# Optimization experiments

Hardware: AMD Instinct MI355X
Metric: run time of the kernel (lower is better)

## Reference

```python
import jax, jax.numpy as jnp
import numpy as np
from jax import lax

V = 9; C1 = 80; C2 = 40; C4 = 24; CH = 32
H1, W1 = 30, 40; H2, W2 = 60, 80; H4, W4 = 120, 160
SHAPE = (96, 96, 96); N = 131072; EPS = 1e-5
OFFS = np.stack(np.meshgrid(np.arange(-1, 2), np.arange(-1, 2), np.arange(-1, 2), indexing='ij'), -1).reshape(-1, 3).astype(np.int32)  # 27 kernel offsets


def conv2d(x, w, b):
    y = lax.conv_general_dilated(x, w, (1, 1), 'SAME', dimension_numbers=('NCHW', 'OIHW', 'NCHW'))
    return y + b[None, :, None, None]


def bn1d(x, g, b):  # eval-mode BatchNorm1d (running_mean=0, running_var=1)
    return g * x * (1.0 / np.sqrt(1.0 + EPS)) + b


def layernorm(x, g, b):
    m = x.mean(-1, keepdims=True)
    v = ((x - m) ** 2).mean(-1, keepdims=True)
    return (x - m) / jnp.sqrt(v + EPS) * g + b


def grid_sample_zeros(img, gx, gy):
    # img [V,C,H,W]; gx,gy [V,M] normalized to [-1,1]; bilinear, align_corners=True, zeros padding
    Vn, C, H, W = img.shape
    px = (gx + 1.0) * 0.5 * (W - 1)
    py = (gy + 1.0) * 0.5 * (H - 1)
    x0 = jnp.floor(px); y0 = jnp.floor(py)
    wx = px - x0; wy = py - y0
    flat = img.reshape(Vn, C, H * W)
    def corner(xc, yc, wgt):
        valid = (xc >= 0) & (xc <= W - 1) & (yc >= 0) & (yc <= H - 1)
        xi = jnp.clip(xc, 0, W - 1).astype(jnp.int32)
        yi = jnp.clip(yc, 0, H - 1).astype(jnp.int32)
        idx = yi * W + xi  # [V,M]
        g = jax.vmap(lambda f, i: f[:, i])(flat, idx)  # [V,C,M]
        return g * (wgt * valid)[:, None, :]
    return (corner(x0, y0, (1 - wx) * (1 - wy)) + corner(x0 + 1, y0, wx * (1 - wy))
            + corner(x0, y0 + 1, (1 - wx) * wy) + corner(x0 + 1, y0 + 1, wx * wy))


def subm_conv(feat, W3, cxyz, grid):
    # submanifold sparse 3x3x3 conv: per-offset gather of active neighbors -> GEMM -> accumulate
    n = feat.shape[0]
    shp = jnp.asarray(SHAPE, jnp.int32)
    out = jnp.zeros((n, W3.shape[-1]), feat.dtype)
    for k in range(27):
        nc = cxyz + jnp.asarray(OFFS[k])
        inb = jnp.all((nc >= 0) & (nc < shp), axis=1)
        ncc = jnp.clip(nc, 0, shp - 1)
        idx = grid[ncc[:, 0], ncc[:, 1], ncc[:, 2]]
        ok = (inb & (idx >= 0)).astype(feat.dtype)
        g = feat[jnp.clip(idx, 0, n - 1)] * ok[:, None]
        out = out + g @ W3[k]
    return out


def _forward(feats_1x, feats_2x, feats_4x, origin, voxel_size, KRcam,
             w_f1, b_f1, w_f2, b_f2, w_f4, b_f4, w_down, b_down,
             w_p1, b_p1, w_p2, b_p2, w_p3, b_p3, w_p4, b_p4,
             bn0_g, bn0_b, w_elan, w_s1, ln1_g, ln1_b, w_s2, ln2_g, ln2_b,
             w_s3, ln3_g, ln3_b, w_s4, bn4_g, bn4_b,
             coords, stage, min_view_number):
    # feat_fusion_pre (bs=1, take batch 0)
    f1 = jax.nn.relu(conv2d(feats_1x[:, 0], w_f1, b_f1))
    f2 = jax.nn.relu(conv2d(feats_2x[:, 0], w_f2, b_f2))
    f4 = jax.nn.relu(conv2d(feats_4x[:, 0], w_f4, b_f4))
    f1 = jax.image.resize(f1, (V, C1, H2, W2), 'bilinear')  # F.interpolate x2
    f4 = f4.reshape(V, C4, H2, 2, W2, 2).mean(axis=(3, 5))  # AvgPool2d(2)
    fuse = jnp.concatenate([f1, f2, f4], axis=1)
    fuse = jax.nn.relu(conv2d(fuse, w_down, b_down))
    for w, b in ((w_p1, b_p1), (w_p2, b_p2), (w_p3, b_p3), (w_p4, b_p4)):
        fuse = fuse + jax.nn.relu(conv2d(fuse, w, b))  # residual blocks -> [V,CH,H2,W2]
    # multi-view projection
    cxyz = coords[:, 1:]
    world = cxyz.astype(jnp.float32) * voxel_size + origin[0]
    hom = jnp.concatenate([world, jnp.ones_like(world[:, :1])], axis=1)  # [N,4]
    im_p = jnp.einsum('vij,nj->vin', KRcam[:, 0], hom)  # [V,3,N]
    im_z = im_p[:, 2]
    gx = 2.0 * (im_p[:, 0] / im_z) / (W4 - 1) - 1.0
    gy = 2.0 * (im_p[:, 1] / im_z) / (H4 - 1) - 1.0
    mask = (jnp.abs(gx) <= 1) & (jnp.abs(gy) <= 1) & (im_z > 0)  # [V,N]
    count = mask.sum(0).astype(jnp.float32)
    # inputs are constructed so every voxel is seen by all views: valid_voxel compaction == identity
    feats = grid_sample_zeros(fuse, gx, gy) * mask[:, None, :]  # [V,CH,N]
    feat = feats.transpose(2, 0, 1)  # [N,V,CH]
    m = mask.T.astype(feat.dtype)  # [N,V]
    den = m.sum(1, keepdims=True)
    mean = (m[..., None] * feat).sum(1) / den
    var = (m[..., None] * (feat - mean[:, None, :]) ** 2).sum(1) / den  # [N,CH]
    # sparse subm conv chain
    sc = cxyz // (2 ** (2 - stage))  # stage=2 -> identity
    grid = jnp.full(SHAPE, -1, jnp.int32).at[sc[:, 0], sc[:, 1], sc[:, 2]].set(jnp.arange(N, dtype=jnp.int32))
    x = bn1d(var, bn0_g, bn0_b)
    x = jax.nn.relu(subm_conv(x, w_elan, sc, grid))  # Spares3dELAN stand-in
    r = jax.nn.relu(subm_conv(x, w_s1, sc, grid)); x = layernorm(r + x, ln1_g, ln1_b)
    r = jax.nn.relu(subm_conv(x, w_s2, sc, grid)); x = layernorm(r + x, ln2_g, ln2_b)
    r = jax.nn.relu(subm_conv(x, w_s3, sc, grid)); x = layernorm(r + x, ln3_g, ln3_b)
    occ = bn1d(subm_conv(x, w_s4, sc, grid), bn4_g, bn4_b)  # [N,1]
    return occ, coords, count


def setup_inputs() -> dict:
    key = jax.random.key(0)
    keys = jax.random.split(key, 40)
    ki = iter(range(40))
    def rn(shape, s=1.0):
        return jax.random.normal(keys[next(ki)], shape, jnp.float32) * s
    inp = {}
    inp['feats_1x'] = rn((V, 1, C1, H1, W1))
    inp['feats_2x'] = rn((V, 1, C2, H2, W2))
    inp['feats_4x'] = rn((V, 1, C4, H4, W4))
    flat = np.arange(N, dtype=np.int64) * 6  # unique active voxels in a 96^3 grid
    cx = flat // (96 * 96); rem = flat % (96 * 96)
    inp['coords'] = jnp.asarray(np.stack([np.zeros(N, np.int64), cx, rem // 96, rem % 96], 1), jnp.int32)
    inp['origin'] = jnp.asarray([[-1.92, -1.92, 1.0]], jnp.float32)
    inp['voxel_size'] = jnp.float32(0.04)
    fx, fy = 38.0, 28.0
    P = np.zeros((V, 1, 3, 4), np.float32)
    for v in range(V):
        P[v, 0] = np.array([[fx, 0.0, (W4 - 1) / 2, fx * 0.02 * (v - 4)],
                            [0.0, fy, (H4 - 1) / 2, 0.0],
                            [0.0, 0.0, 1.0, 0.0]], np.float32)
    inp['KRcam'] = jnp.asarray(P)
    s = 0.05
    inp['w_f1'] = rn((C1, C1, 3, 3), s); inp['b_f1'] = rn((C1,), s)
    inp['w_f2'] = rn((C2, C2, 3, 3), s); inp['b_f2'] = rn((C2,), s)
    inp['w_f4'] = rn((C4, C4, 3, 3), s); inp['b_f4'] = rn((C4,), s)
    inp['w_down'] = rn((CH, C1 + C2 + C4, 1, 1), s); inp['b_down'] = rn((CH,), s)
    for i in (1, 2, 3, 4):
        inp['w_p%d' % i] = rn((CH, CH, 3, 3), s); inp['b_p%d' % i] = rn((CH,), s)
    inp['bn0_g'] = jnp.ones((CH,), jnp.float32); inp['bn0_b'] = jnp.zeros((CH,), jnp.float32)
    inp['w_elan'] = rn((27, CH, CH), s)
    inp['w_s1'] = rn((27, CH, CH), s); inp['ln1_g'] = jnp.ones((CH,), jnp.float32); inp['ln1_b'] = jnp.zeros((CH,), jnp.float32)
    inp['w_s2'] = rn((27, CH, CH), s); inp['ln2_g'] = jnp.ones((CH,), jnp.float32); inp['ln2_b'] = jnp.zeros((CH,), jnp.float32)
    inp['w_s3'] = rn((27, CH, CH), s); inp['ln3_g'] = jnp.ones((CH,), jnp.float32); inp['ln3_b'] = jnp.zeros((CH,), jnp.float32)
    inp['w_s4'] = rn((27, CH, 1), s); inp['bn4_g'] = jnp.ones((1,), jnp.float32); inp['bn4_b'] = jnp.zeros((1,), jnp.float32)
    inp['stage'] = 2
    inp['min_view_number'] = 1
    return inp


def reference(feats_1x, feats_2x, feats_4x, origin, voxel_size, KRcam,
              w_f1, b_f1, w_f2, b_f2, w_f4, b_f4, w_down, b_down,
              w_p1, b_p1, w_p2, b_p2, w_p3, b_p3, w_p4, b_p4,
              bn0_g, bn0_b, w_elan, w_s1, ln1_g, ln1_b, w_s2, ln2_g, ln2_b,
              w_s3, ln3_g, ln3_b, w_s4, bn4_g, bn4_b,
              coords, stage, min_view_number):
    return _forward(feats_1x, feats_2x, feats_4x, origin, voxel_size, KRcam,
                    w_f1, b_f1, w_f2, b_f2, w_f4, b_f4, w_down, b_down,
                    w_p1, b_p1, w_p2, b_p2, w_p3, b_p3, w_p4, b_p4,
                    bn0_g, bn0_b, w_elan, w_s1, ln1_g, ln1_b, w_s2, ln2_g, ln2_b,
                    w_s3, ln3_g, ln3_b, w_s4, bn4_g, bn4_b,
                    coords, stage, min_view_number)
```

## Files before the change

### kernel.cpp

```cpp
#include <hip/hip_runtime.h>
#include <math.h>

#define VN 9
#define NVOX 131072
#define GS 96
static constexpr float INVS = 0.9999950000374997f;

typedef short bf16x8 __attribute__((ext_vector_type(8)));
typedef float f32x4v __attribute__((ext_vector_type(4)));

__device__ inline float4 ld4(const float* p){ return *reinterpret_cast<const float4*>(p); }

__device__ inline ushort f2b(float f){
  unsigned u = __float_as_uint(f);
  unsigned r = (u + 0x7fffu + ((u >> 16) & 1u)) >> 16;
  return (ushort)r;
}
__device__ inline float b2f(ushort s){ return __uint_as_float(((unsigned)s) << 16); }
__device__ inline float blo(unsigned u){ return __uint_as_float(u << 16); }
__device__ inline float bhi(unsigned u){ return __uint_as_float(u & 0xffff0000u); }

__device__ inline float4 ld4b(const ushort* p){
  uint2 u = *reinterpret_cast<const uint2*>(p);
  float4 r; r.x = blo(u.x); r.y = bhi(u.x); r.z = blo(u.y); r.w = bhi(u.y); return r;
}
__device__ inline void st4b(ushort* p, float4 v){
  uint2 u;
  u.x = (unsigned)f2b(v.x) | ((unsigned)f2b(v.y) << 16);
  u.y = (unsigned)f2b(v.z) | ((unsigned)f2b(v.w) << 16);
  *reinterpret_cast<uint2*>(p) = u;
}

__device__ inline void wprep2_dev(const float* __restrict__ w, ushort* __restrict__ o,
                                  int Cout, int Cin, int K, int CK, int CoutPad, int tid){
  int ci32 = tid & 31;
  int co = (tid >> 5) % CoutPad;
  int ck = (tid / (32*CoutPad)) % CK;
  int tap = tid / (32*CoutPad*CK);
  int ci = ck*32 + ci32;
  float v = 0.f;
  if (co < Cout && ci < Cin) v = w[(size_t)(co*Cin + ci)*K*K + tap];
  o[tid] = f2b(v);
}
__device__ inline void wprep_dev(const float* __restrict__ w, ushort* __restrict__ o, int tid){
  int k = tid >> 10;
  int r = tid & 1023;
  int co = r >> 5;
  int ci = r & 31;
  o[tid] = f2b(w[k*1024 + ci*32 + co]);
}

__device__ inline void nhwc_tile_dev(const float* __restrict__ in, ushort* __restrict__ out,
                                     int C, int Cpad, int HW, int tile, int tilesPerV,
                                     float* lds, int tx){
  int v  = tile / tilesPerV;
  int p0 = (tile - v*tilesPerV) * 64;
  const float* ip = in + (size_t)v*C*HW + p0;
  int iters = Cpad >> 2;
  for (int i = 0; i < iters; ++i){
    int idx = i*256 + tx;
    int c = idx >> 6;
    int p = idx & 63;
    float val = 0.f;
    if (c < C && (p0 + p) < HW) val = ip[(size_t)c*HW + p];
    lds[c*65 + p] = val;
  }
  __syncthreads();
  int groups = Cpad >> 2;
  int tot = 64*groups;
  for (int basei = 0; basei < tot; basei += 256){
    int idx = basei + tx;
    if (idx < tot){
      int g  = idx % groups;
      int px = idx / groups;
      if ((p0 + px) < HW){
        float4 r;
        r.x = lds[(g*4+0)*65 + px];
        r.y = lds[(g*4+1)*65 + px];
        r.z = lds[(g*4+2)*65 + px];
        r.w = lds[(g*4+3)*65 + px];
        st4b(out + (size_t)(v*HW + p0 + px)*Cpad + g*4, r);
      }
    }
  }
}

__global__ __launch_bounds__(256) void k_prep(
    const float* wf1s, const float* wf2s, const float* wf4s, const float* wdns,
    const float* wp0s, const float* wp1s, const float* wp2s, const float* wp3s,
    const float* wes, const float* ws1s, const float* ws2s, const float* ws3s,
    ushort* wf1, ushort* wf2, ushort* wf4, ushort* wdn,
    ushort* wp0, ushort* wp1, ushort* wp2, ushort* wp3,
    ushort* w2e, ushort* w2s1, ushort* w2s2, ushort* w2s3,
    int* grid,
    const float* f1, const float* f2, const float* f4,
    ushort* o1, ushort* o2, ushort* o4){
  __shared__ float lds[96*65];
  int bid = blockIdx.x;
  int tx = threadIdx.x;
  if (bid < 270){ int t = bid*256+tx; if (t < 69120) wprep2_dev(wf1s, wf1, 80, 80, 3, 3, 80, t); return; }
  bid -= 270;
  if (bid < 108){ int t = bid*256+tx; if (t < 27648) wprep2_dev(wf2s, wf2, 40, 40, 3, 2, 48, t); return; }
  bid -= 108;
  if (bid < 36){ int t = bid*256+tx; if (t < 9216) wprep2_dev(wf4s, wf4, 24, 24, 3, 1, 32, t); return; }
  bid -= 36;
  if (bid < 20){ int t = bid*256+tx; if (t < 5120) wprep2_dev(wdns, wdn, 32, 144, 1, 5, 32, t); return; }
  bid -= 20;
  if (bid < 36){ int t = bid*256+tx; if (t < 9216) wprep2_dev(wp0s, wp0, 32, 32, 3, 1, 32, t); return; }
  bid -= 36;
  if (bid < 36){ int t = bid*256+tx; if (t < 9216) wprep2_dev(wp1s, wp1, 32, 32, 3, 1, 32, t); return; }
  bid -= 36;
  if (bid < 36){ int t = bid*256+tx; if (t < 9216) wprep2_dev(wp2s, wp2, 32, 32, 3, 1, 32, t); return; }
  bid -= 36;
  if (bid < 36){ int t = bid*256+tx; if (t < 9216) wprep2_dev(wp3s, wp3, 32, 32, 3, 1, 32, t); return; }
  bid -= 36;
  if (bid < 108){ int t = bid*256+tx; if (t < 27648) wprep_dev(wes, w2e, t); return; }
  bid -= 108;
  if (bid < 108){ int t = bid*256+tx; if (t < 27648) wprep_dev(ws1s, w2s1, t); return; }
  bid -= 108;
  if (bid < 108){ int t = bid*256+tx; if (t < 27648) wprep_dev(ws2s, w2s2, t); return; }
  bid -= 108;
  if (bid < 108){ int t = bid*256+tx; if (t < 27648) wprep_dev(ws3s, w2s3, t); return; }
  bid -= 108;
  if (bid < 3456){ int t = bid*256+tx; if (t < GS*GS*GS) grid[t] = -1; return; }
  bid -= 3456;
  if (bid < 171){ nhwc_tile_dev(f1, o1, 80, 96, 1200, bid, 19, lds, tx); return; }
  bid -= 171;
  if (bid < 675){ nhwc_tile_dev(f2, o2, 40, 64, 4800, bid, 75, lds, tx); return; }
  bid -= 675;
  if (bid < 2700){ nhwc_tile_dev(f4, o4, 24, 32, 19200, bid, 300, lds, tx); }
}

template<int CK, int NT, int TAPS, int MT>
__device__ void conv_dev(
    const ushort* __restrict__ fin, const ushort* __restrict__ w2,
    const float* __restrict__ bias, ushort* __restrict__ outp,
    int H, int W, int total, int Cout, int outStride, int outOff,
    const ushort* __restrict__ skipin, int bid, int tid){
  constexpr int CIN = CK*32;
  constexpr int COP = NT*16;
  int lane = tid & 63;
  int wave = tid >> 6;
  int vbase = bid*(MT*64) + wave*(MT*16);
  int m = lane & 15, q = lane >> 4;
  int HW = H*W;
  int p[MT], py[MT], px[MT]; bool pin[MT];
  #pragma unroll
  for (int t = 0; t < MT; ++t){
    int pp = vbase + t*16 + m;
    pin[t] = pp < total;
    if (pp > total-1) pp = total-1;
    p[t] = pp;
    int v = pp / HW; int rem = pp - v*HW;
    int y = rem / W;
    py[t] = y; px[t] = rem - y*W;
  }
  f32x4v acc[MT][NT];
  #pragma unroll
  for (int t = 0; t < MT; ++t)
    #pragma unroll
    for (int n = 0; n < NT; ++n) acc[t][n] = 0.f;
  bf16x8 z = (short)0;

  #pragma unroll 1
  for (int tap = 0; tap < TAPS; ++tap){
    int dy = (TAPS == 9) ? tap/3 - 1 : 0;
    int dx = (TAPS == 9) ? tap%3 - 1 : 0;
    int off = dy*W + dx;
    bool val[MT];
    #pragma unroll
    for (int t = 0; t < MT; ++t)
      val[t] = pin[t] && ((unsigned)(py[t]+dy) < (unsigned)H)
                      && ((unsigned)(px[t]+dx) < (unsigned)W);
    #pragma unroll
    for (int ck = 0; ck < CK; ++ck){
      bf16x8 Af[MT], Bf[NT];
      #pragma unroll
      for (int t = 0; t < MT; ++t){
        size_t idx = val[t] ? (size_t)(p[t]+off) : 0;
        bf16x8 a = *(const bf16x8*)(fin + idx*CIN + ck*32 + q*8);
        Af[t] = val[t] ? a : z;
      }
      #pragma unroll
      for (int n = 0; n < NT; ++n)
        Bf[n] = *(const bf16x8*)(w2 + ((size_t)((tap*CK+ck)*COP + n*16 + m))*32 + q*8);
      #pragma unroll
      for (int t = 0; t < MT; ++t)
        #pragma unroll
        for (int n = 0; n < NT; ++n)
          acc[t][n] = __builtin_amdgcn_mfma_f32_16x16x32_bf16(Af[t], Bf[n], acc[t][n], 0, 0, 0);
    }
  }

  #pragma unroll
  for (int n = 0; n < NT; ++n){
    int co = n*16 + m;
    bool cok = co < Cout;
    float bs = cok ? bias[co] : 0.f;
    #pragma unroll
    for (int t = 0; t < MT; ++t){
      #pragma unroll
      for (int r = 0; r < 4; ++r){
        int pp = vbase + t*16 + q*4 + r;
        if (pp < total && cok){
          float x = fmaxf(acc[t][n][r] + bs, 0.f);
          if (skipin) x += b2f(skipin[(size_t)pp*CIN + co]);
          outp[(size_t)pp*outStride + outOff + co] = f2b(x);
        }
      }
    }
  }
}

template<int CK, int NT, int TAPS, int MT>
__global__ __launch_bounds__(256) void k_conv_mfma(
    const ushort* __restrict__ fin, const ushort* __restrict__ w2,
    const float* __restrict__ bias, ushort* __restrict__ outp,
    int H, int W, int total, int Cout, int outStride, int outOff,
    const ushort* __restrict__ skipin){
  conv_dev<CK,NT,TAPS,MT>(fin, w2, bias, outp, H, W, total, Cout, outStride, outOff,
                          skipin, blockIdx.x, threadIdx.x);
}

template<int TH, int NT>
__device__ void conv_lds_dev(
    const ushort* __restrict__ fin, const ushort* __restrict__ w2,
    const float* __restrict__ bias, ushort* __restrict__ outp,
    int H, int W, int Cout, int outStride,
    const ushort* __restrict__ skipin, ushort* lds, int bid, int tid){
  constexpr int RPW = TH/4;
  constexpr int PS = 36;
  int xtiles = W >> 4;
  int ytiles = (H + TH - 1) / TH;
  int v  = bid / (ytiles*xtiles);
  int rem = bid - v*(ytiles*xtiles);
  int ty = (rem / xtiles) * TH;
  int tx = (rem % xtiles) * 16;
  const ushort* ibase = fin + (size_t)v*H*W*32;
  for (int i = tid; i < (TH+2)*18*4; i += 256){
    int chunk = i & 3;
    int pxi = i >> 2;
    int ly = pxi / 18, lx = pxi - ly*18;
    int gy = ty + ly - 1, gx = tx + lx - 1;
    uint4 d = {0,0,0,0};
    if ((unsigned)gy < (unsigned)H && (unsigned)gx < (unsigned)W)
      d = *(const uint4*)(ibase + ((size_t)gy*W + gx)*32 + chunk*8);
    *(uint4*)(lds + (size_t)(ly*18 + lx)*PS + chunk*8) = d;
  }
  __syncthreads();
  int lane = tid & 63;
  int wave = tid >> 6;
  int m = lane & 15, q = lane >> 4;
  f32x4v acc[RPW][NT];
  #pragma unroll
  for (int t = 0; t < RPW; ++t)
    #pragma unroll
    for (int n = 0; n < NT; ++n) acc[t][n] = 0.f;

  #pragma unroll 1
  for (int tap = 0; tap < 9; ++tap){
    int dy = tap/3 - 1, dx = tap%3 - 1;
    bf16x8 Af[RPW], Bf[NT];
    #pragma unroll
    for (int t = 0; t < RPW; ++t){
      int ly = wave*RPW + t + 1 + dy;
      int lx = m + 1 + dx;
      Af[t] = *(const bf16x8*)(lds + (size_t)(ly*18 + lx)*PS + q*8);
    }
    #pragma unroll
    for (int n = 0; n < NT; ++n)
      Bf[n] = *(const bf16x8*)(w2 + ((size_t)(tap*(NT*16) + n*16 + m))*32 + q*8);
    #pragma unroll
    for (int t = 0; t < RPW; ++t)
      #pragma unroll
      for (int n = 0; n < NT; ++n)
        acc[t][n] = __builtin_amdgcn_mfma_f32_16x16x32_bf16(Af[t], Bf[n], acc[t][n], 0, 0, 0);
  }

  #pragma unroll
  for (int n = 0; n < NT; ++n){
    int co = n*16 + m;
    bool cok = co < Cout;
    float bs = cok ? bias[co] : 0.f;
    #pragma unroll
    for (int t = 0; t < RPW; ++t){
      int y = ty + wave*RPW + t;
      #pragma unroll
      for (int r = 0; r < 4; ++r){
        int x = tx + q*4 + r;
        if (y < H && cok){
          size_t pp = (size_t)(v*H + y)*W + x;
          float val = fmaxf(acc[t][n][r] + bs, 0.f);
          if (skipin) val += b2f(skipin[pp*32 + co]);
          outp[pp*outStride + co] = f2b(val);
        }
      }
    }
  }
}

__global__ __launch_bounds__(256) void k_conv_lds4(
    const ushort* __restrict__ fin, const ushort* __restrict__ w2,
    const float* __restrict__ bias, ushort* __restrict__ outp,
    const ushort* __restrict__ skipin){
  __shared__ ushort lds[6*18*36];
  conv_lds_dev<4,2>(fin, w2, bias, outp, 60, 80, 32, 32, skipin, lds, blockIdx.x, threadIdx.x);
}

__device__ void scatter_dev(const int* __restrict__ coords, const int* __restrict__ stage,
                            int* __restrict__ grid, int* __restrict__ scn,
                            float* __restrict__ coords_out,
                            const float* __restrict__ origin, const float* __restrict__ vsz,
                            const float* __restrict__ KR,
                            uint4* __restrict__ samp, float* __restrict__ cnt, int n){
  int c0 = coords[n*4], c1 = coords[n*4+1], c2 = coords[n*4+2], c3 = coords[n*4+3];
  coords_out[n*4+0] = (float)c0;
  coords_out[n*4+1] = (float)c1;
  coords_out[n*4+2] = (float)c2;
  coords_out[n*4+3] = (float)c3;
  int sh = 2 - stage[0];
  int s1 = c1 >> sh, s2 = c2 >> sh, s3 = c3 >> sh;
  scn[n*3+0] = s1; scn[n*3+1] = s2; scn[n*3+2] = s3;
  grid[(s1*GS + s2)*GS + s3] = n;

  float vs = vsz[0];
  float wx = (float)c1*vs + origin[0];
  float wy = (float)c2*vs + origin[1];
  float wz = (float)c3*vs + origin[2];
  float den = 0.f;
  #pragma unroll 1
  for (int v = 0; v < VN; ++v){
    const float* P = KR + v*12;
    float ix = P[0]*wx + P[1]*wy + P[2]*wz + P[3];
    float iy = P[4]*wx + P[5]*wy + P[6]*wz + P[7];
    float iz = P[8]*wx + P[9]*wy + P[10]*wz + P[11];
    float gx = 2.f*(ix/iz)/159.f - 1.f;
    float gy = 2.f*(iy/iz)/119.f - 1.f;
    bool ok = (fabsf(gx) <= 1.f) && (fabsf(gy) <= 1.f) && (iz > 0.f);
    float px = ok ? (gx + 1.f)*0.5f*79.f : 0.f;
    float py = ok ? (gy + 1.f)*0.5f*59.f : 0.f;
    float x0f = floorf(px), y0f = floorf(py);
    float fx = px - x0f, fy = py - y0f;
    int idx = (int)y0f*80 + (int)x0f;
    float mf = ok ? 1.f : 0.f;
    float w00 = (1.f-fx)*(1.f-fy)*mf, w01 = fx*(1.f-fy)*mf;
    float w10 = (1.f-fx)*fy*mf,       w11 = fx*fy*mf;
    uint4 s;
    s.x = (unsigned)idx;
    s.y = (unsigned)f2b(w00) | ((unsigned)f2b(w01) << 16);
    s.z = (unsigned)f2b(w10) | ((unsigned)f2b(w11) << 16);
    s.w = 0;
    samp[(size_t)v*NVOX + n] = s;
    den += mf;
  }
  cnt[n] = den;
}

__global__ __launch_bounds__(256) void k_heads(
    const ushort* nhwc1, const ushort* wf1, const float* b_f1, ushort* t1,
    const ushort* nhwc2, const ushort* wf2, const float* b_f2, ushort* fcat,
    const ushort* nhwc4, const ushort* wf4, const float* b_f4, ushort* t4,
    const int* coords, const int* stage, int* grid, int* scn, float* coords_out,
    const float* origin, const float* vsz, const float* KR, uint4* samp, float* cnt){
  __shared__ ushort lds[18*18*36];
  int bid = blockIdx.x;
  int tid = threadIdx.x;
  if (bid < 169){ conv_dev<3,5,9,1>(nhwc1, wf1, b_f1, t1, 30, 40, 10800, 80, 80, 0, nullptr, bid, tid); return; }
  bid -= 169;
  if (bid < 720){ conv_lds_dev<16,2>(nhwc4, wf4, b_f4, t4, 120, 160, 24, 24, nullptr, lds, bid, tid); return; }
  bid -= 720;
  if (bid < 675){ conv_dev<2,3,9,1>(nhwc2, wf2, b_f2, fcat, 60, 80, 43200, 40, 160, 80, nullptr, bid, tid); return; }
  bid -= 675;
  { int n = bid*256 + tid;
    scatter_dev(coords, stage, grid, scn, coords_out, origin, vsz, KR, samp, cnt, n); }
}

__global__ __launch_bounds__(256) void k_respool_nbr(
    const ushort* __restrict__ t1, const ushort* __restrict__ t4, ushort* __restrict__ fc,
    const int* __restrict__ scn, const int* __restrict__ grid,
    int* __restrict__ nbr, unsigned* __restrict__ gmask16){
  __shared__ unsigned m16[4];
  int bid = blockIdx.x;
  int tidx = threadIdx.x;
  if (bid < 5063){
    int tid = bid*256 + tidx;
    if (tid < 864000){
      int c4 = tid % 20;
      int x  = (tid / 20) % 80;
      int y  = (tid / 1600) % 60;
      int v  = tid / 96000;
      int c = c4*4;
      int ky = y >> 1; int y0, y1; float wy0, wy1;
      if ((y & 1) == 0){ y0 = ky-1; y1 = ky; wy0 = 0.25f; wy1 = 0.75f; if (y0 < 0){ y0 = 0; wy0 = 0.f; wy1 = 1.f; } }
      else             { y0 = ky; y1 = ky+1; wy0 = 0.75f; wy1 = 0.25f; if (y1 > 29){ y1 = 29; wy1 = 0.f; wy0 = 1.f; } }
      int kx = x >> 1; int x0, x1; float wx0, wx1;
      if ((x & 1) == 0){ x0 = kx-1; x1 = kx; wx0 = 0.25f; wx1 = 0.75f; if (x0 < 0){ x0 = 0; wx0 = 0.f; wx1 = 1.f; } }
      else             { x0 = kx; x1 = kx+1; wx0 = 0.75f; wx1 = 0.25f; if (x1 > 39){ x1 = 39; wx1 = 0.f; wx0 = 1.f; } }
      float4 a00 = ld4b(t1 + ((size_t)(v*30 + y0)*40 + x0)*80 + c);
      float4 a01 = ld4b(t1 + ((size_t)(v*30 + y0)*40 + x1)*80 + c);
      float4 a10 = ld4b(t1 + ((size_t)(v*30 + y1)*40 + x0)*80 + c);
      float4 a11 = ld4b(t1 + ((size_t)(v*30 + y1)*40 + x1)*80 + c);
      float w00 = wy0*wx0, w01 = wy0*wx1, w10 = wy1*wx0, w11 = wy1*wx1;
      float4 r;
      r.x = w00*a00.x + w01*a01.x + w10*a10.x + w11*a11.x;
      r.y = w00*a00.y + w01*a01.y + w10*a10.y + w11*a11.y;
      r.z = w00*a00.z + w01*a01.z + w10*a10.z + w11*a11.z;
      r.w = w00*a00.w + w01*a01.w + w10*a10.w + w11*a11.w;
      st4b(fc + ((size_t)(v*60 + y)*80 + x)*160 + c, r);
      return;
    }
    int t = tid - 864000;
    if (t >= 432000) return;
    int c4 = t % 10;
    int x  = (t / 10) % 80;
    int y  = (t / 800) % 60;
    int v  = t / 48000;
    if (c4 < 6){
      int c = c4*4;
      const ushort* b0 = t4 + ((size_t)(v*120 + 2*y)*160 + 2*x)*24 + c;
      float4 a = ld4b(b0), b = ld4b(b0 + 24), cc = ld4b(b0 + 160*24), d = ld4b(b0 + 160*24 + 24);
      float4 r;
      r.x = 0.25f*(a.x + b.x + cc.x + d.x);
      r.y = 0.25f*(a.y + b.y + cc.y + d.y);
      r.z = 0.25f*(a.z + b.z + cc.z + d.z);
      r.w = 0.25f*(a.w + b.w + cc.w + d.w);
      st4b(fc + ((size_t)(v*60 + y)*80 + x)*160 + 120 + c, r);
    } else {
      float4 zz = {0.f,0.f,0.f,0.f};
      st4b(fc + ((size_t)(v*60 + y)*80 + x)*160 + 144 + (c4-6)*4, zz);
    }
    return;
  }
  bid -= 5063;
  if (tidx < 4) m16[tidx] = 0;
  __syncthreads();
  int vb = bid*64;
  int lane = tidx & 63;
  int wv = tidx >> 6;
  int n = vb + lane;
  int sx = scn[n*3+0], sy = scn[n*3+1], sz = scn[n*3+2];
  int k0 = wv*7;
  int k1 = min(27, k0 + 7);
  unsigned msk = 0;
  #pragma unroll 1
  for (int k = k0; k < k1; ++k){
    int dx = k/9 - 1, dy = (k/3)%3 - 1, dz = k%3 - 1;
    int nx = sx+dx, ny = sy+dy, nz = sz+dz;
    int idx = -1;
    if (((unsigned)nx < 96u) && ((unsigned)ny < 96u) && ((unsigned)nz < 96u))
      idx = grid[(nx*GS + ny)*GS + nz];
    nbr[(size_t)k*NVOX + n] = idx;
    unsigned long long b = __ballot(idx >= 0);
    unsigned sub = (unsigned)((b >> ((lane >> 4)*16)) & 0xFFFFull);
    if (sub) msk |= (1u << k);
  }
  if ((lane & 15) == 0 && msk) atomicOr(&m16[lane >> 4], msk);
  __syncthreads();
  if (tidx < 4) gmask16[(vb >> 4) + tidx] = m16[tidx];
}

__global__ __launch_bounds__(256) void k_sample(
    const ushort* __restrict__ fuse, const uint4* __restrict__ samp,
    const float* __restrict__ cnt, const float* __restrict__ bn0g,
    const float* __restrict__ bn0b, ushort* __restrict__ F0){
  int tid = blockIdx.x*256 + threadIdx.x;
  int vox = tid >> 3;
  int c4 = tid & 7;
  int c = c4*4;
  float s0=0.f,s1=0.f,s2=0.f,s3=0.f;
  float q0=0.f,q1=0.f,q2=0.f,q3=0.f;
  uint4 sv = samp[vox];
  #pragma unroll 1
  for (int v = 0; v < VN; ++v){
    uint4 svn = sv;
    if (v+1 < VN) svn = samp[(size_t)(v+1)*NVOX + vox];
    float w00 = blo(sv.y), w01 = bhi(sv.y);
    float w10 = blo(sv.z), w11 = bhi(sv.z);
    const ushort* bp = fuse + (size_t)v*153600 + (size_t)sv.x*32 + c;
    float4 a00 = ld4b(bp);
    float4 a01 = ld4b(bp + 32);
    float4 a10 = ld4b(bp + 2560);
    float4 a11 = ld4b(bp + 2592);
    float g0 = w00*a00.x + w01*a01.x + w10*a10.x + w11*a11.x;
    float g1 = w00*a00.y + w01*a01.y + w10*a10.y + w11*a11.y;
    float g2 = w00*a00.z + w01*a01.z + w10*a10.z + w11*a11.z;
    float g3 = w00*a00.w + w01*a01.w + w10*a10.w + w11*a11.w;
    s0 += g0; q0 += g0*g0;
    s1 += g1; q1 += g1*g1;
    s2 += g2; q2 += g2*g2;
    s3 += g3; q3 += g3*g3;
    sv = svn;
  }
  float iden = 1.f/cnt[vox];
  float m0 = s0*iden, m1 = s1*iden, m2 = s2*iden, m3 = s3*iden;
  float4 g = ld4(bn0g + c);
  float4 b = ld4(bn0b + c);
  float4 r;
  r.x = g.x*fmaxf(q0*iden - m0*m0, 0.f)*INVS + b.x;
  r.y = g.y*fmaxf(q1*iden - m1*m1, 0.f)*INVS + b.y;
  r.z = g.z*fmaxf(q2*iden - m2*m2, 0.f)*INVS + b.z;
  r.w = g.w*fmaxf(q3*iden - m3*m3, 0.f)*INVS + b.w;
  st4b(F0 + (size_t)vox*32 + c, r);
}

template<int MODE>
__global__ __launch_bounds__(256, 8) void k_subm_mfma(
    const ushort* __restrict__ fin, const ushort* __restrict__ w2,
    const int* __restrict__ nbr, const unsigned* __restrict__ gmask16,
    const float* __restrict__ lng, const float* __restrict__ lnb,
    ushort* __restrict__ fout){
  int lane = threadIdx.x & 63;
  int wave = threadIdx.x >> 6;
  int vb = blockIdx.x*64 + wave*16;
  int m = lane & 15;
  int q = lane >> 4;

  f32x4v acc0 = 0.f, acc1 = 0.f;
  bf16x8 zc = (short)0;
  unsigned rem = gmask16[vb >> 4];
  int k0 = -1, k1 = -1;
  int id0 = -1, id1 = -1;
  if (rem){ k0 = __ffs(rem) - 1; rem &= rem - 1; id0 = nbr[(size_t)k0*NVOX + vb + m]; }
  if (rem){ k1 = __ffs(rem) - 1; rem &= rem - 1; id1 = nbr[(size_t)k1*NVOX + vb + m]; }
  bf16x8 A0 = zc;
  if (k0 >= 0){
    bf16x8 a = *(const bf16x8*)(fin + (size_t)(id0 < 0 ? 0 : id0)*32 + q*8);
    A0 = (id0 < 0) ? zc : a;
  }
  while (k0 >= 0){
    bf16x8 A1 = zc;
    if (k1 >= 0){
      bf16x8 a = *(const bf16x8*)(fin + (size_t)(id1 < 0 ? 0 : id1)*32 + q*8);
      A1 = (id1 < 0) ? zc : a;
    }
    int k2 = -1, id2 = -1;
    if (rem){ k2 = __ffs(rem) - 1; rem &= rem - 1; id2 = nbr[(size_t)k2*NVOX + vb + m]; }
    bf16x8 b0 = *(const bf16x8*)(w2 + (size_t)(k0*32 + m)*32 + q*8);
    bf16x8 b1 = *(const bf16x8*)(w2 + (size_t)(k0*32 + 16 + m)*32 + q*8);
    acc0 = __builtin_amdgcn_mfma_f32_16x16x32_bf16(A0, b0, acc0, 0, 0, 0);
    acc1 = __builtin_amdgcn_mfma_f32_16x16x32_bf16(A0, b1, acc1, 0, 0, 0);
    A0 = A1; id1 = id2; k0 = k1; k1 = k2;
  }

  int ch0 = m, ch1 = 16 + m;
  float g0 = 0.f, g1 = 0.f, bb0 = 0.f, bb1 = 0.f;
  if (MODE == 1){ g0 = lng[ch0]; g1 = lng[ch1]; bb0 = lnb[ch0]; bb1 = lnb[ch1]; }
  #pragma unroll
  for (int r = 0; r < 4; ++r){
    int vox = vb + q*4 + r;
    float x0 = fmaxf(acc0[r], 0.f);
    float x1 = fmaxf(acc1[r], 0.f);
    if (MODE == 1){
      x0 += b2f(fin[(size_t)vox*32 + ch0]);
      x1 += b2f(fin[(size_t)vox*32 + ch1]);
      float s = x0 + x1;
      s += __shfl_xor(s, 1, 16);
      s += __shfl_xor(s, 2, 16);
      s += __shfl_xor(s, 4, 16);
      s += __shfl_xor(s, 8, 16);
      float mean = s * (1.f/32.f);
      float d0 = x0 - mean, d1 = x1 - mean;
      float v2 = d0*d0 + d1*d1;
      v2 += __shfl_xor(v2, 1, 16);
      v2 += __shfl_xor(v2, 2, 16);
      v2 += __shfl_xor(v2, 4, 16);
      v2 += __shfl_xor(v2, 8, 16);
      float rs = 1.f / sqrtf(v2*(1.f/32.f) + 1e-5f);
      x0 = d0*rs*g0 + bb0;
      x1 = d1*rs*g1 + bb1;
    }
    fout[(size_t)vox*32 + ch0] = f2b(x0);
    fout[(size_t)vox*32 + ch1] = f2b(x1);
  }
}

__global__ __launch_bounds__(256) void k_s4(
    const ushort* __restrict__ fin, const float* __restrict__ w4,
    const int* __restrict__ nbr, const unsigned* __restrict__ gmask16,
    const float* __restrict__ bn4g, const float* __restrict__ bn4b,
    float* __restrict__ occ){
  int n = blockIdx.x*256 + threadIdx.x;
  if (n >= NVOX) return;
  unsigned rem = gmask16[n >> 4];
  float acc = 0.f;
  int k = -1, idx = -1;
  if (rem){ k = __ffs(rem) - 1; rem &= rem - 1; idx = nbr[(size_t)k*NVOX + n]; }
  while (k >= 0){
    int k2 = -1, idx2 = -1;
    if (rem){ k2 = __ffs(rem) - 1; rem &= rem - 1; idx2 = nbr[(size_t)k2*NVOX + n]; }
    if (idx >= 0){
      const uint4* r4 = (const uint4*)(fin + (size_t)idx*32);
      const float* wk = w4 + k*32;
      #pragma unroll
      for (int u = 0; u < 4; ++u){
        uint4 d = r4[u];
        const float* w8 = wk + u*8;
        acc += blo(d.x)*w8[0] + bhi(d.x)*w8[1];
        acc += blo(d.y)*w8[2] + bhi(d.y)*w8[3];
        acc += blo(d.z)*w8[4] + bhi(d.z)*w8[5];
        acc += blo(d.w)*w8[6] + bhi(d.w)*w8[7];
      }
    }
    k = k2; idx = idx2;
  }
  occ[n] = bn4g[0]*acc*INVS + bn4b[0];
}

extern "C" void kernel_launch(void* const* d_in, const int* in_sizes, int n_in,
                              void* d_out, int out_size, void* d_ws, size_t ws_size,
                              hipStream_t stream){
  const float* feats1 = (const float*)d_in[0];
  const float* feats2 = (const float*)d_in[1];
  const float* feats4 = (const float*)d_in[2];
  const int*   coords = (const int*)d_in[3];
  const float* origin = (const float*)d_in[4];
  const float* vsz    = (const float*)d_in[5];
  const float* KR     = (const float*)d_in[6];
  const float* w_f1 = (const float*)d_in[7];  const float* b_f1 = (const float*)d_in[8];
  const float* w_f2 = (const float*)d_in[9];  const float* b_f2 = (const float*)d_in[10];
  const float* w_f4 = (const float*)d_in[11]; const float* b_f4 = (const float*)d_in[12];
  const float* w_dn = (const float*)d_in[13]; const float* b_dn = (const float*)d_in[14];
  const float* w_p[4] = {(const float*)d_in[15], (const float*)d_in[17],
                         (const float*)d_in[19], (const float*)d_in[21]};
  const float* b_p[4] = {(const float*)d_in[16], (const float*)d_in[18],
                         (const float*)d_in[20], (const float*)d_in[22]};
  const float* bn0g = (const float*)d_in[23]; const float* bn0b = (const float*)d_in[24];
  const float* w_elan = (const float*)d_in[25];
  const float* w_s1 = (const float*)d_in[26]; const float* ln1g = (const float*)d_in[27]; const float* ln1b = (const float*)d_in[28];
  const float* w_s2 = (const float*)d_in[29]; const float* ln2g = (const float*)d_in[30]; const float* ln2b = (const float*)d_in[31];
  const float* w_s3 = (const float*)d_in[32]; const float* ln3g = (const float*)d_in[33]; const float* ln3b = (const float*)d_in[34];
  const float* w_s4 = (const float*)d_in[35]; const float* bn4g = (const float*)d_in[36]; const float* bn4b = (const float*)d_in[37];
  const int* stage  = (const int*)d_in[38];
  float* out = (float*)d_out;
  char* base = (char*)d_ws;

  size_t off = 0;
  auto alloc = [&](size_t bytes)->char*{ char* p = base + off; off += (bytes + 255) & ~(size_t)255; return p; };
  ushort* nhwc1 = (ushort*)alloc((size_t)9*30*40*96*2);
  ushort* nhwc2 = (ushort*)alloc((size_t)9*60*80*64*2);
  ushort* nhwc4 = (ushort*)alloc((size_t)9*120*160*32*2);
  ushort* t1    = (ushort*)alloc((size_t)9*30*40*80*2);
  ushort* t4    = (ushort*)alloc((size_t)9*120*160*24*2);
  ushort* fcat  = (ushort*)alloc((size_t)9*60*80*160*2);
  ushort* A     = (ushort*)alloc((size_t)9*60*80*32*2);
  ushort* B     = (ushort*)alloc((size_t)9*60*80*32*2);
  ushort* Fb0   = (ushort*)alloc((size_t)NVOX*32*2);
  ushort* Fb1   = (ushort*)alloc((size_t)NVOX*32*2);
  int*    nbr   = (int*)alloc((size_t)27*NVOX*4);
  int*    grid  = (int*)alloc((size_t)GS*GS*GS*4);
  int*    scn   = (int*)alloc((size_t)NVOX*3*4);
  unsigned* gmask16 = (unsigned*)alloc((size_t)(NVOX/16)*4);
  ushort* wf1   = (ushort*)alloc(9*3*80*32*2);
  ushort* wf2   = (ushort*)alloc(9*2*48*32*2);
  ushort* wf4   = (ushort*)alloc(9*1*32*32*2);
  ushort* wdn   = (ushort*)alloc(1*5*32*32*2);
  ushort* wp0   = (ushort*)alloc(9*1*32*32*2);
  ushort* wp1   = (ushort*)alloc(9*1*32*32*2);
  ushort* wp2   = (ushort*)alloc(9*1*32*32*2);
  ushort* wp3   = (ushort*)alloc(9*1*32*32*2);
  ushort* w2e   = (ushort*)alloc(27*1024*2);
  ushort* w2s1  = (ushort*)alloc(27*1024*2);
  ushort* w2s2  = (ushort*)alloc(27*1024*2);
  ushort* w2s3  = (ushort*)alloc(27*1024*2);
  uint4* samp = (uint4*)alloc((size_t)VN*NVOX*16);

  auto nb = [](int total){ return (total + 255)/256; };

  k_prep<<<8012,256,0,stream>>>(
      w_f1, w_f2, w_f4, w_dn, w_p[0], w_p[1], w_p[2], w_p[3],
      w_elan, w_s1, w_s2, w_s3,
      wf1, wf2, wf4, wdn, wp0, wp1, wp2, wp3, w2e, w2s1, w2s2, w2s3, grid,
      feats1, feats2, feats4, nhwc1, nhwc2, nhwc4);

  k_heads<<<169 + 720 + 675 + 512,256,0,stream>>>(
      nhwc1, wf1, b_f1, t1,
      nhwc2, wf2, b_f2, fcat,
      nhwc4, wf4, b_f4, t4,
      coords, stage, grid, scn, out + NVOX,
      origin, vsz, KR, samp, out + 5*NVOX);

  k_respool_nbr<<<5063 + 2048,256,0,stream>>>(t1, t4, fcat, scn, grid, nbr, gmask16);

  k_conv_mfma<5,2,1,1><<<675,256,0,stream>>>(fcat, wdn, b_dn, A, 60, 80, 43200, 32, 32, 0, nullptr);
  k_conv_lds4<<<675,256,0,stream>>>(A, wp0, b_p[0], B, A);
  k_conv_lds4<<<675,256,0,stream>>>(B, wp1, b_p[1], A, B);
  k_conv_lds4<<<675,256,0,stream>>>(A, wp2, b_p[2], B, A);
  k_conv_lds4<<<675,256,0,stream>>>(B, wp3, b_p[3], A, B);

  k_sample<<<NVOX/32,256,0,stream>>>(A, samp, out + 5*NVOX, bn0g, bn0b, Fb0);

  k_subm_mfma<0><<<NVOX/64,256,0,stream>>>(Fb0, w2e,  nbr, gmask16, nullptr, nullptr, Fb1);
  k_subm_mfma<1><<<NVOX/64,256,0,stream>>>(Fb1, w2s1, nbr, gmask16, ln1g, ln1b, Fb0);
  k_subm_mfma<1><<<NVOX/64,256,0,stream>>>(Fb0, w2s2, nbr, gmask16, ln2g, ln2b, Fb1);
  k_subm_mfma<1><<<NVOX/64,256,0,stream>>>(Fb1, w2s3, nbr, gmask16, ln3g, ln3b, Fb0);

  k_s4<<<nb(NVOX),256,0,stream>>>(Fb0, w_s4, nbr, gmask16, bn4g, bn4b, out);
}
```

Measured before the change: 355.1 us.

## Process 32 voxels per wave in sparse conv, compact sampling data, skip empty nbr writes

The submanifold MFMA conv now handles two 16-voxel tiles per wave. Each weight fragment load feeds four MFMAs instead of two, and the offset loop runs over the union of both tiles' masks. Grid size halves and the occupancy hint drops from 8 to 4. Sampling metadata is split into a 16-bit index array and an 8-byte weight array instead of a 16-byte record, which cuts traffic. Neighbour-table writes are skipped for offsets with no active neighbour in a 16-voxel group. Those entries are now never read, because every reader checks the per-tile mask first.

After: 347.6 us. 1.02x faster.

```diff
diff --git a/kernel.cpp b/kernel.cpp
--- a/kernel.cpp
+++ b/kernel.cpp
@@ -312,7 +312,8 @@
                             float* __restrict__ coords_out,
                             const float* __restrict__ origin, const float* __restrict__ vsz,
                             const float* __restrict__ KR,
-                            uint4* __restrict__ samp, float* __restrict__ cnt, int n){
+                            ushort* __restrict__ sidx, uint2* __restrict__ sw,
+                            float* __restrict__ cnt, int n){
   int c0 = coords[n*4], c1 = coords[n*4+1], c2 = coords[n*4+2], c3 = coords[n*4+3];
   coords_out[n*4+0] = (float)c0;
   coords_out[n*4+1] = (float)c1;
@@ -345,12 +346,11 @@
     float mf = ok ? 1.f : 0.f;
     float w00 = (1.f-fx)*(1.f-fy)*mf, w01 = fx*(1.f-fy)*mf;
     float w10 = (1.f-fx)*fy*mf,       w11 = fx*fy*mf;
-    uint4 s;
-    s.x = (unsigned)idx;
-    s.y = (unsigned)f2b(w00) | ((unsigned)f2b(w01) << 16);
-    s.z = (unsigned)f2b(w10) | ((unsigned)f2b(w11) << 16);
-    s.w = 0;
-    samp[(size_t)v*NVOX + n] = s;
+    uint2 s;
+    s.x = (unsigned)f2b(w00) | ((unsigned)f2b(w01) << 16);
+    s.y = (unsigned)f2b(w10) | ((unsigned)f2b(w11) << 16);
+    sidx[(size_t)v*NVOX + n] = (ushort)idx;
+    sw[(size_t)v*NVOX + n] = s;
     den += mf;
   }
   cnt[n] = den;
@@ -361,7 +361,8 @@
     const ushort* nhwc2, const ushort* wf2, const float* b_f2, ushort* fcat,
     const ushort* nhwc4, const ushort* wf4, const float* b_f4, ushort* t4,
     const int* coords, const int* stage, int* grid, int* scn, float* coords_out,
-    const float* origin, const float* vsz, const float* KR, uint4* samp, float* cnt){
+    const float* origin, const float* vsz, const float* KR,
+    ushort* sidx, uint2* sw, float* cnt){
   __shared__ ushort lds[18*18*36];
   int bid = blockIdx.x;
   int tid = threadIdx.x;
@@ -372,7 +373,7 @@
   if (bid < 675){ conv_dev<2,3,9,1>(nhwc2, wf2, b_f2, fcat, 60, 80, 43200, 40, 160, 80, nullptr, bid, tid); return; }
   bid -= 675;
   { int n = bid*256 + tid;
-    scatter_dev(coords, stage, grid, scn, coords_out, origin, vsz, KR, samp, cnt, n); }
+    scatter_dev(coords, stage, grid, scn, coords_out, origin, vsz, KR, sidx, sw, cnt, n); }
 }
 
 __global__ __launch_bounds__(256) void k_respool_nbr(
@@ -449,10 +450,12 @@
     int idx = -1;
     if (((unsigned)nx < 96u) && ((unsigned)ny < 96u) && ((unsigned)nz < 96u))
       idx = grid[(nx*GS + ny)*GS + nz];
-    nbr[(size_t)k*NVOX + n] = idx;
     unsigned long long b = __ballot(idx >= 0);
     unsigned sub = (unsigned)((b >> ((lane >> 4)*16)) & 0xFFFFull);
-    if (sub) msk |= (1u << k);
+    if (sub){
+      nbr[(size_t)k*NVOX + n] = idx;
+      msk |= (1u << k);
+    }
   }
   if ((lane & 15) == 0 && msk) atomicOr(&m16[lane >> 4], msk);
   __syncthreads();
@@ -460,7 +463,8 @@
 }
 
 __global__ __launch_bounds__(256) void k_sample(
-    const ushort* __restrict__ fuse, const uint4* __restrict__ samp,
+    const ushort* __restrict__ fuse, const ushort* __restrict__ sidx,
+    const uint2* __restrict__ sw,
     const float* __restrict__ cnt, const float* __restrict__ bn0g,
     const float* __restrict__ bn0b, ushort* __restrict__ F0){
   int tid = blockIdx.x*256 + threadIdx.x;
@@ -469,14 +473,18 @@
   int c = c4*4;
   float s0=0.f,s1=0.f,s2=0.f,s3=0.f;
   float q0=0.f,q1=0.f,q2=0.f,q3=0.f;
-  uint4 sv = samp[vox];
+  ushort si = sidx[vox];
+  uint2 wv = sw[vox];
   #pragma unroll 1
   for (int v = 0; v < VN; ++v){
-    uint4 svn = sv;
-    if (v+1 < VN) svn = samp[(size_t)(v+1)*NVOX + vox];
-    float w00 = blo(sv.y), w01 = bhi(sv.y);
-    float w10 = blo(sv.z), w11 = bhi(sv.z);
-    const ushort* bp = fuse + (size_t)v*153600 + (size_t)sv.x*32 + c;
+    ushort sn = si; uint2 wn = wv;
+    if (v+1 < VN){
+      sn = sidx[(size_t)(v+1)*NVOX + vox];
+      wn = sw[(size_t)(v+1)*NVOX + vox];
+    }
+    float w00 = blo(wv.x), w01 = bhi(wv.x);
+    float w10 = blo(wv.y), w11 = bhi(wv.y);
+    const ushort* bp = fuse + (size_t)v*153600 + (size_t)si*32 + c;
     float4 a00 = ld4b(bp);
     float4 a01 = ld4b(bp + 32);
     float4 a10 = ld4b(bp + 2560);
@@ -489,7 +497,7 @@
     s1 += g1; q1 += g1*g1;
     s2 += g2; q2 += g2*g2;
     s3 += g3; q3 += g3*g3;
-    sv = svn;
+    si = sn; wv = wn;
   }
   float iden = 1.f/cnt[vox];
   float m0 = s0*iden, m1 = s1*iden, m2 = s2*iden, m3 = s3*iden;
@@ -504,73 +512,91 @@
 }
 
 template<int MODE>
-__global__ __launch_bounds__(256, 8) void k_subm_mfma(
+__global__ __launch_bounds__(256, 4) void k_subm_mfma(
     const ushort* __restrict__ fin, const ushort* __restrict__ w2,
     const int* __restrict__ nbr, const unsigned* __restrict__ gmask16,
     const float* __restrict__ lng, const float* __restrict__ lnb,
     ushort* __restrict__ fout){
   int lane = threadIdx.x & 63;
   int wave = threadIdx.x >> 6;
-  int vb = blockIdx.x*64 + wave*16;
+  int vb = blockIdx.x*128 + wave*32;
   int m = lane & 15;
   int q = lane >> 4;
 
-  f32x4v acc0 = 0.f, acc1 = 0.f;
+  unsigned rem0 = gmask16[(vb >> 4) + 0];
+  unsigned rem1 = gmask16[(vb >> 4) + 1];
+  unsigned rem = rem0 | rem1;
+
+  f32x4v acc[2][2];
+  acc[0][0] = 0.f; acc[0][1] = 0.f; acc[1][0] = 0.f; acc[1][1] = 0.f;
   bf16x8 zc = (short)0;
-  unsigned rem = gmask16[vb >> 4];
+
   int k0 = -1, k1 = -1;
-  int id0 = -1, id1 = -1;
-  if (rem){ k0 = __ffs(rem) - 1; rem &= rem - 1; id0 = nbr[(size_t)k0*NVOX + vb + m]; }
-  if (rem){ k1 = __ffs(rem) - 1; rem &= rem - 1; id1 = nbr[(size_t)k1*NVOX + vb + m]; }
-  bf16x8 A0 = zc;
+  int a0 = -1, b0 = -1, a1 = -1, b1 = -1;
+  if (rem){ k0 = __ffs(rem) - 1; rem &= rem - 1;
+            a0 = ((rem0 >> k0) & 1) ? nbr[(size_t)k0*NVOX + vb + m] : -1;
+            b0 = ((rem1 >> k0) & 1) ? nbr[(size_t)k0*NVOX + vb + 16 + m] : -1; }
+  if (rem){ k1 = __ffs(rem) - 1; rem &= rem - 1;
+            a1 = ((rem0 >> k1) & 1) ? nbr[(size_t)k1*NVOX + vb + m] : -1;
+            b1 = ((rem1 >> k1) & 1) ? nbr[(size_t)k1*NVOX + vb + 16 + m] : -1; }
+  bf16x8 A0 = zc, B0 = zc;
   if (k0 >= 0){
-    bf16x8 a = *(const bf16x8*)(fin + (size_t)(id0 < 0 ? 0 : id0)*32 + q*8);
-    A0 = (id0 < 0) ? zc : a;
+    bf16x8 t;
+    t = *(const bf16x8*)(fin + (size_t)(a0 < 0 ? 0 : a0)*32 + q*8); A0 = (a0 < 0) ? zc : t;
+    t = *(const bf16x8*)(fin + (size_t)(b0 < 0 ? 0 : b0)*32 + q*8); B0 = (b0 < 0) ? zc : t;
   }
   while (k0 >= 0){
-    bf16x8 A1 = zc;
+    bf16x8 A1 = zc, B1 = zc;
     if (k1 >= 0){
-      bf16x8 a = *(const bf16x8*)(fin + (size_t)(id1 < 0 ? 0 : id1)*32 + q*8);
-      A1 = (id1 < 0) ? zc : a;
-    }
-    int k2 = -1, id2 = -1;
-    if (rem){ k2 = __ffs(rem) - 1; rem &= rem - 1; id2 = nbr[(size_t)k2*NVOX + vb + m]; }
-    bf16x8 b0 = *(const bf16x8*)(w2 + (size_t)(k0*32 + m)*32 + q*8);
-    bf16x8 b1 = *(const bf16x8*)(w2 + (size_t)(k0*32 + 16 + m)*32 + q*8);
-    acc0 = __builtin_amdgcn_mfma_f32_16x16x32_bf16(A0, b0, acc0, 0, 0, 0);
-    acc1 = __builtin_amdgcn_mfma_f32_16x16x32_bf16(A0, b1, acc1, 0, 0, 0);
-    A0 = A1; id1 = id2; k0 = k1; k1 = k2;
+      bf16x8 t;
+      t = *(const bf16x8*)(fin + (size_t)(a1 < 0 ? 0 : a1)*32 + q*8); A1 = (a1 < 0) ? zc : t;
+      t = *(const bf16x8*)(fin + (size_t)(b1 < 0 ? 0 : b1)*32 + q*8); B1 = (b1 < 0) ? zc : t;
+    }
+    int k2 = -1, a2 = -1, b2 = -1;
+    if (rem){ k2 = __ffs(rem) - 1; rem &= rem - 1;
+              a2 = ((rem0 >> k2) & 1) ? nbr[(size_t)k2*NVOX + vb + m] : -1;
+              b2 = ((rem1 >> k2) & 1) ? nbr[(size_t)k2*NVOX + vb + 16 + m] : -1; }
+    bf16x8 w0 = *(const bf16x8*)(w2 + (size_t)(k0*32 + m)*32 + q*8);
+    bf16x8 w1 = *(const bf16x8*)(w2 + (size_t)(k0*32 + 16 + m)*32 + q*8);
+    acc[0][0] = __builtin_amdgcn_mfma_f32_16x16x32_bf16(A0, w0, acc[0][0], 0, 0, 0);
+    acc[0][1] = __builtin_amdgcn_mfma_f32_16x16x32_bf16(A0, w1, acc[0][1], 0, 0, 0);
+    acc[1][0] = __builtin_amdgcn_mfma_f32_16x16x32_bf16(B0, w0, acc[1][0], 0, 0, 0);
+    acc[1][1] = __builtin_amdgcn_mfma_f32_16x16x32_bf16(B0, w1, acc[1][1], 0, 0, 0);
+    A0 = A1; B0 = B1; a1 = a2; b1 = b2; k0 = k1; k1 = k2;
   }
 
   int ch0 = m, ch1 = 16 + m;
   float g0 = 0.f, g1 = 0.f, bb0 = 0.f, bb1 = 0.f;
   if (MODE == 1){ g0 = lng[ch0]; g1 = lng[ch1]; bb0 = lnb[ch0]; bb1 = lnb[ch1]; }
   #pragma unroll
-  for (int r = 0; r < 4; ++r){
-    int vox = vb + q*4 + r;
-    float x0 = fmaxf(acc0[r], 0.f);
-    float x1 = fmaxf(acc1[r], 0.f);
-    if (MODE == 1){
-      x0 += b2f(fin[(size_t)vox*32 + ch0]);
-      x1 += b2f(fin[(size_t)vox*32 + ch1]);
-      float s = x0 + x1;
-      s += __shfl_xor(s, 1, 16);
-      s += __shfl_xor(s, 2, 16);
-      s += __shfl_xor(s, 4, 16);
-      s += __shfl_xor(s, 8, 16);
-      float mean = s * (1.f/32.f);
-      float d0 = x0 - mean, d1 = x1 - mean;
-      float v2 = d0*d0 + d1*d1;
-      v2 += __shfl_xor(v2, 1, 16);
-      v2 += __shfl_xor(v2, 2, 16);
-      v2 += __shfl_xor(v2, 4, 16);
-      v2 += __shfl_xor(v2, 8, 16);
-      float rs = 1.f / sqrtf(v2*(1.f/32.f) + 1e-5f);
-      x0 = d0*rs*g0 + bb0;
-      x1 = d1*rs*g1 + bb1;
-    }
-    fout[(size_t)vox*32 + ch0] = f2b(x0);
-    fout[(size_t)vox*32 + ch1] = f2b(x1);
+  for (int t = 0; t < 2; ++t){
+    #pragma unroll
+    for (int r = 0; r < 4; ++r){
+      int vox = vb + t*16 + q*4 + r;
+      float x0 = fmaxf(acc[t][0][r], 0.f);
+      float x1 = fmaxf(acc[t][1][r], 0.f);
+      if (MODE == 1){
+        x0 += b2f(fin[(size_t)vox*32 + ch0]);
+        x1 += b2f(fin[(size_t)vox*32 + ch1]);
+        float s = x0 + x1;
+        s += __shfl_xor(s, 1, 16);
+        s += __shfl_xor(s, 2, 16);
+        s += __shfl_xor(s, 4, 16);
+        s += __shfl_xor(s, 8, 16);
+        float mean = s * (1.f/32.f);
+        float d0 = x0 - mean, d1 = x1 - mean;
+        float v2 = d0*d0 + d1*d1;
+        v2 += __shfl_xor(v2, 1, 16);
+        v2 += __shfl_xor(v2, 2, 16);
+        v2 += __shfl_xor(v2, 4, 16);
+        v2 += __shfl_xor(v2, 8, 16);
+        float rs = 1.f / sqrtf(v2*(1.f/32.f) + 1e-5f);
+        x0 = d0*rs*g0 + bb0;
+        x1 = d1*rs*g1 + bb1;
+      }
+      fout[(size_t)vox*32 + ch0] = f2b(x0);
+      fout[(size_t)vox*32 + ch1] = f2b(x1);
+    }
   }
 }
 
@@ -662,7 +688,8 @@
   ushort* w2s1  = (ushort*)alloc(27*1024*2);
   ushort* w2s2  = (ushort*)alloc(27*1024*2);
   ushort* w2s3  = (ushort*)alloc(27*1024*2);
-  uint4* samp = (uint4*)alloc((size_t)VN*NVOX*16);
+  ushort* sidx  = (ushort*)alloc((size_t)VN*NVOX*2);
+  uint2*  sw    = (uint2*)alloc((size_t)VN*NVOX*8);
 
   auto nb = [](int total){ return (total + 255)/256; };
 
@@ -677,7 +704,7 @@
       nhwc2, wf2, b_f2, fcat,
       nhwc4, wf4, b_f4, t4,
       coords, stage, grid, scn, out + NVOX,
-      origin, vsz, KR, samp, out + 5*NVOX);
+      origin, vsz, KR, sidx, sw, out + 5*NVOX);
 
   k_respool_nbr<<<5063 + 2048,256,0,stream>>>(t1, t4, fcat, scn, grid, nbr, gmask16);
 
@@ -687,12 +714,12 @@
   k_conv_lds4<<<675,256,0,stream>>>(A, wp2, b_p[2], B, A);
   k_conv_lds4<<<675,256,0,stream>>>(B, wp3, b_p[3], A, B);
 
-  k_sample<<<NVOX/32,256,0,stream>>>(A, samp, out + 5*NVOX, bn0g, bn0b, Fb0);
-
-  k_subm_mfma<0><<<NVOX/64,256,0,stream>>>(Fb0, w2e,  nbr, gmask16, nullptr, nullptr, Fb1);
-  k_subm_mfma<1><<<NVOX/64,256,0,stream>>>(Fb1, w2s1, nbr, gmask16, ln1g, ln1b, Fb0);
-  k_subm_mfma<1><<<NVOX/64,256,0,stream>>>(Fb0, w2s2, nbr, gmask16, ln2g, ln2b, Fb1);
-  k_subm_mfma<1><<<NVOX/64,256,0,stream>>>(Fb1, w2s3, nbr, gmask16, ln3g, ln3b, Fb0);
+  k_sample<<<NVOX/32,256,0,stream>>>(A, sidx, sw, out + 5*NVOX, bn0g, bn0b, Fb0);
+
+  k_subm_mfma<0><<<NVOX/128,256,0,stream>>>(Fb0, w2e,  nbr, gmask16, nullptr, nullptr, Fb1);
+  k_subm_mfma<1><<<NVOX/128,256,0,stream>>>(Fb1, w2s1, nbr, gmask16, ln1g, ln1b, Fb0);
+  k_subm_mfma<1><<<NVOX/128,256,0,stream>>>(Fb0, w2s2, nbr, gmask16, ln2g, ln2b, Fb1);
+  k_subm_mfma<1><<<NVOX/128,256,0,stream>>>(Fb1, w2s3, nbr, gmask16, ln3g, ln3b, Fb0);
 
   k_s4<<<nb(NVOX),256,0,stream>>>(Fb0, w_s4, nbr, gmask16, bn4g, bn4b, out);
 }
```
